# Kernel tuning notes

Measured on AMD Instinct MI355X. Metric: run time of the kernel, lower is better.

The kernel has to match this reference:

```python
import jax, jax.numpy as jnp
import numpy as np

WS = 8          # window_size
NH = 4          # num_heads
C = 128         # embed_dim
HD = C // NH    # head_dim
HID = 4 * C     # mlp hidden
EPS = 1e-5


def _rel_pos_index(ws):
    coords = np.stack(np.meshgrid(np.arange(ws), np.arange(ws), indexing='ij')).reshape(2, -1)
    rel = coords[:, :, None] - coords[:, None, :]          # (2, N, N)
    rel = rel.transpose(1, 2, 0).astype(np.int64)          # (N, N, 2)
    rel[..., 0] += ws - 1
    rel[..., 1] += ws - 1
    rel[..., 0] *= 2 * ws - 1
    return rel.sum(-1)                                     # (N, N)


def _layernorm(x, g, b):
    mu = jnp.mean(x, axis=-1, keepdims=True)
    var = jnp.mean(jnp.square(x - mu), axis=-1, keepdims=True)
    return (x - mu) * jax.lax.rsqrt(var + EPS) * g + b


def setup_inputs() -> dict:
    key = jax.random.key(0)
    ks = jax.random.split(key, 12)
    B, L = 32, 4096
    s = 0.02
    return {
        'x': jax.random.normal(ks[0], (B, L, C), jnp.float32),
        'W_qkv': jax.random.normal(ks[1], (C, 3 * C), jnp.float32) * s,
        'b_qkv': jnp.zeros((3 * C,), jnp.float32),
        'W_out': jax.random.normal(ks[2], (C, C), jnp.float32) * s,
        'b_out': jnp.zeros((C,), jnp.float32),
        'bias_table': jax.random.normal(ks[3], ((2 * WS - 1) ** 2, NH), jnp.float32) * s,
        'g1': jnp.ones((C,), jnp.float32), 'be1': jnp.zeros((C,), jnp.float32),
        'g2': jnp.ones((C,), jnp.float32), 'be2': jnp.zeros((C,), jnp.float32),
        'W_fc1': jax.random.normal(ks[4], (C, HID), jnp.float32) * s,
        'b_fc1': jnp.zeros((HID,), jnp.float32),
        'W_fc2': jax.random.normal(ks[5], (HID, C), jnp.float32) * s,
        'b_fc2': jnp.zeros((C,), jnp.float32),
        'H': 64, 'W': 64,
    }


def reference(x, W_qkv, b_qkv, W_out, b_out, bias_table, g1, be1, g2, be2,
              W_fc1, b_fc1, W_fc2, b_fc2, H, W):
    B, L, _ = x.shape
    N = WS * WS
    shortcut = x
    xn = _layernorm(x, g1, be1)
    # window partition: (B,H,W,C) -> (B*nw, N, C)
    xw = xn.reshape(B, H // WS, WS, W // WS, WS, C)
    xw = xw.transpose(0, 1, 3, 2, 4, 5).reshape(-1, N, C)
    # attention
    qkv = (xw @ W_qkv + b_qkv).reshape(-1, N, 3, NH, HD)
    q, k, v = jnp.moveaxis(qkv, 2, 0)                      # each (Bw, N, NH, HD)
    attn = jnp.einsum('bnhd,bmhd->bhnm', q, k) * (HD ** -0.5)
    idx = jnp.asarray(_rel_pos_index(WS))                  # (N, N)
    bias = bias_table[idx].transpose(2, 0, 1)              # (NH, N, N)
    attn = jax.nn.softmax((attn + bias[None]).astype(jnp.float32), axis=-1).astype(x.dtype)
    o = jnp.einsum('bhnm,bmhd->bnhd', attn, v).reshape(-1, N, C)
    o = o @ W_out + b_out
    # window reverse
    o = o.reshape(B, H // WS, W // WS, WS, WS, C)
    o = o.transpose(0, 1, 3, 2, 4, 5).reshape(B, L, C)
    x = shortcut + o
    # MLP block
    xn = _layernorm(x, g2, be2)
    h = jax.nn.gelu(xn @ W_fc1 + b_fc1, approximate=False)
    return x + (h @ W_fc2 + b_fc2)
```

## Files before the change

### kernel.cpp

```cpp
#include <hip/hip_runtime.h>
#include <hip/hip_bf16.h>

typedef __bf16 bf16;
typedef __bf16 bf16x8 __attribute__((ext_vector_type(8)));
typedef float f32x4 __attribute__((ext_vector_type(4)));

#define C_DIM 128
#define LDA 136
#define LDQ 40
#define LDVT 72
#define LDP 72
#define LDH 264

__device__ __forceinline__ f32x4 mfma16(bf16x8 a, bf16x8 b, f32x4 c) {
  return __builtin_amdgcn_mfma_f32_16x16x32_bf16(a, b, c, 0, 0, 0);
}


__global__ __launch_bounds__(256, 2) void swin_fused(
    const float* __restrict__ x,
    const bf16*  __restrict__ Wqkv_t, const float* __restrict__ b_qkv,
    const bf16*  __restrict__ Wout_t, const float* __restrict__ b_out,
    const float* __restrict__ btabx,
    const float* __restrict__ g1, const float* __restrict__ be1,
    const float* __restrict__ g2, const float* __restrict__ be2,
    const bf16*  __restrict__ Wfc1_t, const float* __restrict__ b_fc1,
    const bf16*  __restrict__ Wfc2_t, const float* __restrict__ b_fc2,
    float* __restrict__ out)
{
  __shared__ __attribute__((aligned(16))) char smem[76800];
  bf16 (*sA)[LDA]       = (bf16(*)[LDA])(smem);
  bf16 (*sQ)[64][LDQ]   = (bf16(*)[64][LDQ])(smem + 17408);
  bf16 (*sK)[64][LDQ]   = (bf16(*)[64][LDQ])(smem + 37888);
  bf16 (*sVT)[32][LDVT] = (bf16(*)[32][LDVT])(smem + 58368);
  bf16 (*sP)[64][LDP]   = (bf16(*)[64][LDP])(smem + 17408);
  bf16 (*sY)[LDA]       = (bf16(*)[LDA])(smem + 17408);
  bf16 (*sH)[LDH]       = (bf16(*)[LDH])(smem + 17408);

  const int tid = threadIdx.x;
  const int w   = tid >> 6;
  const int l   = tid & 63;
  const int l15 = l & 15;
  const int lhi = l >> 4;

  const int win = blockIdx.x;
  const int b   = win >> 6;
  const int wy  = (win >> 3) & 7;
  const int wx  = win & 7;
  const int rowbase = b * 4096 + wy * 512 + wx * 8;

  float yreg[2][4][4];

  {
    const int tok = tid >> 2, seg = tid & 3;
    const int t = rowbase + (tok >> 3) * 64 + (tok & 7);
    const float* xr = x + (size_t)t * C_DIM + seg * 32;
    float f[32]; float s = 0.f, s2 = 0.f;
    #pragma unroll
    for (int i = 0; i < 8; i++) {
      f32x4 v = *(const f32x4*)(xr + i * 4);
      #pragma unroll
      for (int j = 0; j < 4; j++) { float a = v[j]; f[i*4+j] = a; s += a; s2 += a*a; }
    }
    s  += __shfl_xor(s, 1);  s  += __shfl_xor(s, 2);
    s2 += __shfl_xor(s2, 1); s2 += __shfl_xor(s2, 2);
    float mu = s * (1.f/128.f);
    float rs = rsqrtf(s2 * (1.f/128.f) - mu*mu + 1e-5f);
    #pragma unroll
    for (int i = 0; i < 4; i++) {
      f32x4 gv0 = *(const f32x4*)(g1  + seg*32 + i*8);
      f32x4 gv1 = *(const f32x4*)(g1  + seg*32 + i*8 + 4);
      f32x4 bv0 = *(const f32x4*)(be1 + seg*32 + i*8);
      f32x4 bv1 = *(const f32x4*)(be1 + seg*32 + i*8 + 4);
      bf16x8 o;
      #pragma unroll
      for (int j = 0; j < 4; j++) {
        o[j]   = (bf16)((f[i*8+j]   - mu) * rs * gv0[j] + bv0[j]);
        o[j+4] = (bf16)((f[i*8+j+4] - mu) * rs * gv1[j] + bv1[j]);
      }
      *(bf16x8*)&sA[tok][seg*32 + i*8] = o;
    }
  }
  __syncthreads();

  {
    bf16x8 a[4][4];
    #pragma unroll
    for (int mt = 0; mt < 4; mt++)
      #pragma unroll
      for (int ks = 0; ks < 4; ks++)
        a[mt][ks] = *(const bf16x8*)&sA[mt*16 + l15][ks*32 + lhi*8];
    const float scale = 0.17677669529663687f;
    #pragma unroll
    for (int nti = 0; nti < 6; nti++) {
      const int kind = nti >> 1;
      const int d    = (nti & 1) * 16 + l15;
      const int colg = kind * 128 + w * 32 + d;
      const bf16* wp = Wqkv_t + (size_t)colg * 128 + lhi * 8;
      bf16x8 bw[4];
      #pragma unroll
      for (int ks = 0; ks < 4; ks++) bw[ks] = *(const bf16x8*)(wp + ks * 32);
      const float bias = b_qkv[colg];
      #pragma unroll
      for (int mt = 0; mt < 4; mt++) {
        f32x4 acc = {0.f, 0.f, 0.f, 0.f};
        #pragma unroll
        for (int ks = 0; ks < 4; ks++) acc = mfma16(a[mt][ks], bw[ks], acc);
        #pragma unroll
        for (int r = 0; r < 4; r++) {
          const int token = mt*16 + lhi*4 + r;
          float v = acc[r] + bias;
          if (kind == 0)      sQ[w][token][d] = (bf16)(v * scale);
          else if (kind == 1) sK[w][token][d] = (bf16)v;
          else                sVT[w][d][token] = (bf16)v;
        }
      }
    }
  }

  {
    const int h = w;
    bf16x8 aq[4], bk[4];
    #pragma unroll
    for (int mt = 0; mt < 4; mt++) aq[mt] = *(const bf16x8*)&sQ[h][mt*16 + l15][lhi*8];
    #pragma unroll
    for (int ct = 0; ct < 4; ct++) bk[ct] = *(const bf16x8*)&sK[h][ct*16 + l15][lhi*8];
    f32x4 sc[4][4];
    #pragma unroll
    for (int mt = 0; mt < 4; mt++)
      #pragma unroll
      for (int ct = 0; ct < 4; ct++) {
        f32x4 z = {0.f, 0.f, 0.f, 0.f};
        sc[mt][ct] = mfma16(aq[mt], bk[ct], z);
      }
    __syncthreads();
    #pragma unroll
    for (int mt = 0; mt < 4; mt++) {
      #pragma unroll
      for (int r = 0; r < 4; r++) {
        const int n = mt*16 + lhi*4 + r;
        f32x4 bv = *(const f32x4*)(btabx + (((h*64 + n)*16 + l15) << 2));
        float rv[4]; float sum = 0.f;
        #pragma unroll
        for (int ct = 0; ct < 4; ct++) { rv[ct] = __expf(sc[mt][ct][r] + bv[ct]); sum += rv[ct]; }
        #pragma unroll
        for (int o = 1; o < 16; o <<= 1) sum += __shfl_xor(sum, o);
        const float inv = 1.f / sum;
        #pragma unroll
        for (int ct = 0; ct < 4; ct++) sP[h][n][ct*16 + l15] = (bf16)(rv[ct] * inv);
      }
    }
    f32x4 o_[4][2];
    #pragma unroll
    for (int mt = 0; mt < 4; mt++) { f32x4 z = {0.f,0.f,0.f,0.f}; o_[mt][0] = z; o_[mt][1] = z; }
    #pragma unroll
    for (int ks = 0; ks < 2; ks++) {
      bf16x8 ap[4], bvv[2];
      #pragma unroll
      for (int mt = 0; mt < 4; mt++) ap[mt] = *(const bf16x8*)&sP[h][mt*16 + l15][ks*32 + lhi*8];
      #pragma unroll
      for (int c2 = 0; c2 < 2; c2++) bvv[c2] = *(const bf16x8*)&sVT[h][c2*16 + l15][ks*32 + lhi*8];
      #pragma unroll
      for (int mt = 0; mt < 4; mt++)
        #pragma unroll
        for (int c2 = 0; c2 < 2; c2++) o_[mt][c2] = mfma16(ap[mt], bvv[c2], o_[mt][c2]);
    }
    #pragma unroll
    for (int mt = 0; mt < 4; mt++)
      #pragma unroll
      for (int c2 = 0; c2 < 2; c2++)
        #pragma unroll
        for (int r = 0; r < 4; r++)
          sA[mt*16 + lhi*4 + r][h*32 + c2*16 + l15] = (bf16)o_[mt][c2][r];
  }
  __syncthreads();

  {
    bf16x8 a[4][4];
    #pragma unroll
    for (int mt = 0; mt < 4; mt++)
      #pragma unroll
      for (int ks = 0; ks < 4; ks++)
        a[mt][ks] = *(const bf16x8*)&sA[mt*16 + l15][ks*32 + lhi*8];
    #pragma unroll
    for (int nto = 0; nto < 2; nto++) {
      const int col = (w*2 + nto) * 16 + l15;
      const bf16* wp = Wout_t + (size_t)col * 128 + lhi * 8;
      bf16x8 bw[4];
      #pragma unroll
      for (int ks = 0; ks < 4; ks++) bw[ks] = *(const bf16x8*)(wp + ks * 32);
      const float bo = b_out[col];
      #pragma unroll
      for (int mt = 0; mt < 4; mt++) {
        f32x4 acc = {0.f, 0.f, 0.f, 0.f};
        #pragma unroll
        for (int ks = 0; ks < 4; ks++) acc = mfma16(a[mt][ks], bw[ks], acc);
        #pragma unroll
        for (int r = 0; r < 4; r++) {
          const int token = mt*16 + lhi*4 + r;
          const int t = rowbase + (token >> 3) * 64 + (token & 7);
          float v = acc[r] + bo + x[(size_t)t * C_DIM + col];
          yreg[nto][mt][r] = v;
          sY[token][col] = (bf16)v;
        }
      }
    }
  }
  __syncthreads();

  {
    const int tok = tid >> 2, seg = tid & 3;
    float f[32]; float s = 0.f, s2 = 0.f;
    #pragma unroll
    for (int i = 0; i < 4; i++) {
      bf16x8 v = *(const bf16x8*)&sY[tok][seg*32 + i*8];
      #pragma unroll
      for (int j = 0; j < 8; j++) { float a = (float)v[j]; f[i*8+j] = a; s += a; s2 += a*a; }
    }
    s  += __shfl_xor(s, 1);  s  += __shfl_xor(s, 2);
    s2 += __shfl_xor(s2, 1); s2 += __shfl_xor(s2, 2);
    float mu = s * (1.f/128.f);
    float rs = rsqrtf(s2 * (1.f/128.f) - mu*mu + 1e-5f);
    #pragma unroll
    for (int i = 0; i < 4; i++) {
      f32x4 gv0 = *(const f32x4*)(g2  + seg*32 + i*8);
      f32x4 gv1 = *(const f32x4*)(g2  + seg*32 + i*8 + 4);
      f32x4 bv0 = *(const f32x4*)(be2 + seg*32 + i*8);
      f32x4 bv1 = *(const f32x4*)(be2 + seg*32 + i*8 + 4);
      bf16x8 o;
      #pragma unroll
      for (int j = 0; j < 4; j++) {
        o[j]   = (bf16)((f[i*8+j]   - mu) * rs * gv0[j] + bv0[j]);
        o[j+4] = (bf16)((f[i*8+j+4] - mu) * rs * gv1[j] + bv1[j]);
      }
      *(bf16x8*)&sA[tok][seg*32 + i*8] = o;
    }
  }
  __syncthreads();

  {
    bf16x8 a[4][4];
    #pragma unroll
    for (int mt = 0; mt < 4; mt++)
      #pragma unroll
      for (int ks = 0; ks < 4; ks++)
        a[mt][ks] = *(const bf16x8*)&sA[mt*16 + l15][ks*32 + lhi*8];
    f32x4 accF[2][4];
    #pragma unroll
    for (int i = 0; i < 2; i++)
      #pragma unroll
      for (int mt = 0; mt < 4; mt++) { f32x4 z = {0.f,0.f,0.f,0.f}; accF[i][mt] = z; }

    #pragma unroll
    for (int hf = 0; hf < 2; hf++) {
      #pragma unroll
      for (int nti = 0; nti < 4; nti++) {
        const int ntg    = hf*16 + w*4 + nti;
        const int colh   = ntg*16 + l15;
        const int colloc = (w*4 + nti)*16 + l15;
        const bf16* wp = Wfc1_t + (size_t)colh * 128 + lhi * 8;
        bf16x8 bw[4];
        #pragma unroll
        for (int ks = 0; ks < 4; ks++) bw[ks] = *(const bf16x8*)(wp + ks * 32);
        const float bb = b_fc1[colh];
        #pragma unroll
        for (int mt = 0; mt < 4; mt++) {
          f32x4 acc = {0.f, 0.f, 0.f, 0.f};
          #pragma unroll
          for (int ks = 0; ks < 4; ks++) acc = mfma16(a[mt][ks], bw[ks], acc);
          #pragma unroll
          for (int r = 0; r < 4; r++) {
            float v = acc[r] + bb;
            float g = v / (1.f + __expf(-1.702f * v));
            sH[mt*16 + lhi*4 + r][colloc] = (bf16)g;
          }
        }
      }
      __syncthreads();
      #pragma unroll
      for (int ks = 0; ks < 8; ks++) {
        bf16x8 ah[4];
        #pragma unroll
        for (int mt = 0; mt < 4; mt++) ah[mt] = *(const bf16x8*)&sH[mt*16 + l15][ks*32 + lhi*8];
        #pragma unroll
        for (int nto = 0; nto < 2; nto++) {
          bf16x8 bw2 = *(const bf16x8*)(Wfc2_t + (size_t)((w*2 + nto)*16 + l15) * 512 + hf*256 + ks*32 + lhi*8);
          #pragma unroll
          for (int mt = 0; mt < 4; mt++) accF[nto][mt] = mfma16(ah[mt], bw2, accF[nto][mt]);
        }
      }
      __syncthreads();
    }
    #pragma unroll
    for (int nto = 0; nto < 2; nto++) {
      const int col = (w*2 + nto)*16 + l15;
      const float bb = b_fc2[col];
      #pragma unroll
      for (int mt = 0; mt < 4; mt++)
        #pragma unroll
        for (int r = 0; r < 4; r++) {
          const int token = mt*16 + lhi*4 + r;
          const int t = rowbase + (token >> 3) * 64 + (token & 7);
          out[(size_t)t * C_DIM + col] = accF[nto][mt][r] + bb + yreg[nto][mt][r];
        }
    }
  }
}

__global__ void prep_transpose(
    const float* __restrict__ Wqkv, const float* __restrict__ Wout,
    const float* __restrict__ Wfc1, const float* __restrict__ Wfc2,
    const float* __restrict__ btab,
    bf16* __restrict__ Wqkv_t, bf16* __restrict__ Wout_t,
    bf16* __restrict__ Wfc1_t, bf16* __restrict__ Wfc2_t,
    float* __restrict__ btabx)
{
  int i = blockIdx.x * 256 + threadIdx.x;
  if (i < 49152) { int n = i >> 7, k = i & 127; Wqkv_t[i] = (bf16)Wqkv[k*384 + n]; return; }
  i -= 49152;
  if (i < 16384) { int n = i >> 7, k = i & 127; Wout_t[i] = (bf16)Wout[k*128 + n]; return; }
  i -= 16384;
  if (i < 65536) { int n = i >> 7, k = i & 127; Wfc1_t[i] = (bf16)Wfc1[k*512 + n]; return; }
  i -= 65536;
  if (i < 65536) { int n = i >> 9, k = i & 511; Wfc2_t[i] = (bf16)Wfc2[k*128 + n]; return; }
  i -= 65536;
  if (i < 16384) {
    int ct  = i & 3;
    int l15 = (i >> 2) & 15;
    int n   = (i >> 6) & 63;
    int h   = i >> 12;
    int m = ct * 16 + l15;
    int nr = n >> 3, nc = n & 7, mr = m >> 3, mc = m & 7;
    int idx = (nr - mr + 7) * 15 + (nc - mc + 7);
    btabx[i] = btab[idx * 4 + h];
  }
}

extern "C" void kernel_launch(void* const* d_in, const int* in_sizes, int n_in,
                              void* d_out, int out_size, void* d_ws, size_t ws_size,
                              hipStream_t stream)
{
  const float* x    = (const float*)d_in[0];
  const float* Wqkv = (const float*)d_in[1];
  const float* bqkv = (const float*)d_in[2];
  const float* Wout = (const float*)d_in[3];
  const float* bout = (const float*)d_in[4];
  const float* btab = (const float*)d_in[5];
  const float* g1   = (const float*)d_in[6];
  const float* be1  = (const float*)d_in[7];
  const float* g2   = (const float*)d_in[8];
  const float* be2  = (const float*)d_in[9];
  const float* Wfc1 = (const float*)d_in[10];
  const float* bfc1 = (const float*)d_in[11];
  const float* Wfc2 = (const float*)d_in[12];
  const float* bfc2 = (const float*)d_in[13];

  bf16* ws = (bf16*)d_ws;
  bf16* Wqkv_t = ws;
  bf16* Wout_t = ws + 49152;
  bf16* Wfc1_t = ws + 65536;
  bf16* Wfc2_t = ws + 131072;
  float* btabx = (float*)(ws + 196608);

  prep_transpose<<<832, 256, 0, stream>>>(Wqkv, Wout, Wfc1, Wfc2, btab,
                                          Wqkv_t, Wout_t, Wfc1_t, Wfc2_t, btabx);

  const int B = in_sizes[0] / (4096 * 128);
  swin_fused<<<dim3(B * 64), 256, 0, stream>>>(
      x, Wqkv_t, bqkv, Wout_t, bout, btabx, g1, be1, g2, be2,
      Wfc1_t, bfc1, Wfc2_t, bfc2, (float*)d_out);
}
```

Measured before the change: 167.6 us.

## Swap MFMA operand order so accumulators hold contiguous columns for vector stores

Every MFMA now takes the weight or K/V fragment as the A operand and the activation as the B operand. Each lane's four accumulator values then cover four consecutive output columns for a single token rather than four tokens. This turns the per-element bf16 stores to shared memory and the fp32 residual loads and output stores into 4-wide vector accesses, and lets biases load as f32x4. The softmax row reduction becomes two cross-lane shuffles, and the bias table is re-laid out to match the new fragment mapping. The V transpose store remains scalar.

```diff
diff --git a/kernel.cpp b/kernel.cpp
--- a/kernel.cpp
+++ b/kernel.cpp
@@ -3,6 +3,7 @@
 
 typedef __bf16 bf16;
 typedef __bf16 bf16x8 __attribute__((ext_vector_type(8)));
+typedef __bf16 bf16x4 __attribute__((ext_vector_type(4)));
 typedef float f32x4 __attribute__((ext_vector_type(4)));
 
 #define C_DIM 128
@@ -49,7 +50,7 @@
   const int wx  = win & 7;
   const int rowbase = b * 4096 + wy * 512 + wx * 8;
 
-  float yreg[2][4][4];
+  f32x4 yreg[2][4];
 
   {
     const int tok = tid >> 2, seg = tid & 3;
@@ -93,26 +94,35 @@
     const float scale = 0.17677669529663687f;
     #pragma unroll
     for (int nti = 0; nti < 6; nti++) {
-      const int kind = nti >> 1;
-      const int d    = (nti & 1) * 16 + l15;
-      const int colg = kind * 128 + w * 32 + d;
-      const bf16* wp = Wqkv_t + (size_t)colg * 128 + lhi * 8;
+      const int kind  = nti >> 1;
+      const int dhalf = nti & 1;
+      const int colg_l = kind*128 + w*32 + dhalf*16 + l15;
+      const bf16* wp = Wqkv_t + (size_t)colg_l * 128 + lhi * 8;
       bf16x8 bw[4];
       #pragma unroll
       for (int ks = 0; ks < 4; ks++) bw[ks] = *(const bf16x8*)(wp + ks * 32);
-      const float bias = b_qkv[colg];
+      const int colg_o = kind*128 + w*32 + dhalf*16 + lhi*4;
+      f32x4 bias4 = *(const f32x4*)(b_qkv + colg_o);
+      const int d_base = dhalf*16 + lhi*4;
       #pragma unroll
       for (int mt = 0; mt < 4; mt++) {
         f32x4 acc = {0.f, 0.f, 0.f, 0.f};
         #pragma unroll
-        for (int ks = 0; ks < 4; ks++) acc = mfma16(a[mt][ks], bw[ks], acc);
-        #pragma unroll
-        for (int r = 0; r < 4; r++) {
-          const int token = mt*16 + lhi*4 + r;
-          float v = acc[r] + bias;
-          if (kind == 0)      sQ[w][token][d] = (bf16)(v * scale);
-          else if (kind == 1) sK[w][token][d] = (bf16)v;
-          else                sVT[w][d][token] = (bf16)v;
+        for (int ks = 0; ks < 4; ks++) acc = mfma16(bw[ks], a[mt][ks], acc);
+        const int token = mt*16 + l15;
+        if (kind == 0) {
+          bf16x4 v4;
+          #pragma unroll
+          for (int r = 0; r < 4; r++) v4[r] = (bf16)((acc[r] + bias4[r]) * scale);
+          *(bf16x4*)&sQ[w][token][d_base] = v4;
+        } else if (kind == 1) {
+          bf16x4 v4;
+          #pragma unroll
+          for (int r = 0; r < 4; r++) v4[r] = (bf16)(acc[r] + bias4[r]);
+          *(bf16x4*)&sK[w][token][d_base] = v4;
+        } else {
+          #pragma unroll
+          for (int r = 0; r < 4; r++) sVT[w][d_base + r][token] = (bf16)(acc[r] + bias4[r]);
         }
       }
     }
@@ -120,58 +130,67 @@
 
   {
     const int h = w;
-    bf16x8 aq[4], bk[4];
-    #pragma unroll
-    for (int mt = 0; mt < 4; mt++) aq[mt] = *(const bf16x8*)&sQ[h][mt*16 + l15][lhi*8];
-    #pragma unroll
-    for (int ct = 0; ct < 4; ct++) bk[ct] = *(const bf16x8*)&sK[h][ct*16 + l15][lhi*8];
+    bf16x8 qf[4], kf[4];
+    #pragma unroll
+    for (int ctq = 0; ctq < 4; ctq++) qf[ctq] = *(const bf16x8*)&sQ[h][ctq*16 + l15][lhi*8];
+    #pragma unroll
+    for (int kt = 0; kt < 4; kt++) kf[kt] = *(const bf16x8*)&sK[h][kt*16 + l15][lhi*8];
     f32x4 sc[4][4];
     #pragma unroll
-    for (int mt = 0; mt < 4; mt++)
-      #pragma unroll
-      for (int ct = 0; ct < 4; ct++) {
+    for (int ctq = 0; ctq < 4; ctq++)
+      #pragma unroll
+      for (int kt = 0; kt < 4; kt++) {
         f32x4 z = {0.f, 0.f, 0.f, 0.f};
-        sc[mt][ct] = mfma16(aq[mt], bk[ct], z);
+        sc[ctq][kt] = mfma16(kf[kt], qf[ctq], z);
       }
     __syncthreads();
     #pragma unroll
-    for (int mt = 0; mt < 4; mt++) {
-      #pragma unroll
-      for (int r = 0; r < 4; r++) {
-        const int n = mt*16 + lhi*4 + r;
-        f32x4 bv = *(const f32x4*)(btabx + (((h*64 + n)*16 + l15) << 2));
-        float rv[4]; float sum = 0.f;
-        #pragma unroll
-        for (int ct = 0; ct < 4; ct++) { rv[ct] = __expf(sc[mt][ct][r] + bv[ct]); sum += rv[ct]; }
-        #pragma unroll
-        for (int o = 1; o < 16; o <<= 1) sum += __shfl_xor(sum, o);
-        const float inv = 1.f / sum;
-        #pragma unroll
-        for (int ct = 0; ct < 4; ct++) sP[h][n][ct*16 + l15] = (bf16)(rv[ct] * inv);
-      }
-    }
-    f32x4 o_[4][2];
-    #pragma unroll
-    for (int mt = 0; mt < 4; mt++) { f32x4 z = {0.f,0.f,0.f,0.f}; o_[mt][0] = z; o_[mt][1] = z; }
+    for (int ctq = 0; ctq < 4; ctq++) {
+      const int q = ctq*16 + l15;
+      float e[4][4]; float loc = 0.f;
+      #pragma unroll
+      for (int kt = 0; kt < 4; kt++) {
+        f32x4 bt = *(const f32x4*)(btabx + (size_t)(((h*64 + q)*16 + kt*4 + lhi) << 2));
+        #pragma unroll
+        for (int r = 0; r < 4; r++) { e[kt][r] = __expf(sc[ctq][kt][r] + bt[r]); loc += e[kt][r]; }
+      }
+      loc += __shfl_xor(loc, 16);
+      loc += __shfl_xor(loc, 32);
+      const float inv = 1.f / loc;
+      #pragma unroll
+      for (int kt = 0; kt < 4; kt++) {
+        bf16x4 p4;
+        #pragma unroll
+        for (int r = 0; r < 4; r++) p4[r] = (bf16)(e[kt][r] * inv);
+        *(bf16x4*)&sP[h][q][kt*16 + lhi*4] = p4;
+      }
+    }
+    f32x4 o_[2][4];
+    #pragma unroll
+    for (int c2 = 0; c2 < 2; c2++)
+      #pragma unroll
+      for (int ctq = 0; ctq < 4; ctq++) { f32x4 z = {0.f,0.f,0.f,0.f}; o_[c2][ctq] = z; }
     #pragma unroll
     for (int ks = 0; ks < 2; ks++) {
-      bf16x8 ap[4], bvv[2];
-      #pragma unroll
-      for (int mt = 0; mt < 4; mt++) ap[mt] = *(const bf16x8*)&sP[h][mt*16 + l15][ks*32 + lhi*8];
-      #pragma unroll
-      for (int c2 = 0; c2 < 2; c2++) bvv[c2] = *(const bf16x8*)&sVT[h][c2*16 + l15][ks*32 + lhi*8];
-      #pragma unroll
-      for (int mt = 0; mt < 4; mt++)
-        #pragma unroll
-        for (int c2 = 0; c2 < 2; c2++) o_[mt][c2] = mfma16(ap[mt], bvv[c2], o_[mt][c2]);
-    }
-    #pragma unroll
-    for (int mt = 0; mt < 4; mt++)
+      bf16x8 vf[2], pq[4];
+      #pragma unroll
+      for (int c2 = 0; c2 < 2; c2++) vf[c2] = *(const bf16x8*)&sVT[h][c2*16 + l15][ks*32 + lhi*8];
+      #pragma unroll
+      for (int ctq = 0; ctq < 4; ctq++) pq[ctq] = *(const bf16x8*)&sP[h][ctq*16 + l15][ks*32 + lhi*8];
       #pragma unroll
       for (int c2 = 0; c2 < 2; c2++)
         #pragma unroll
-        for (int r = 0; r < 4; r++)
-          sA[mt*16 + lhi*4 + r][h*32 + c2*16 + l15] = (bf16)o_[mt][c2][r];
+        for (int ctq = 0; ctq < 4; ctq++) o_[c2][ctq] = mfma16(vf[c2], pq[ctq], o_[c2][ctq]);
+    }
+    #pragma unroll
+    for (int c2 = 0; c2 < 2; c2++)
+      #pragma unroll
+      for (int ctq = 0; ctq < 4; ctq++) {
+        bf16x4 o4;
+        #pragma unroll
+        for (int r = 0; r < 4; r++) o4[r] = (bf16)o_[c2][ctq][r];
+        *(bf16x4*)&sA[ctq*16 + l15][h*32 + c2*16 + lhi*4] = o4;
+      }
   }
   __syncthreads();
 
@@ -184,25 +203,26 @@
         a[mt][ks] = *(const bf16x8*)&sA[mt*16 + l15][ks*32 + lhi*8];
     #pragma unroll
     for (int nto = 0; nto < 2; nto++) {
-      const int col = (w*2 + nto) * 16 + l15;
-      const bf16* wp = Wout_t + (size_t)col * 128 + lhi * 8;
+      const int col_l = (w*2 + nto) * 16 + l15;
+      const bf16* wp = Wout_t + (size_t)col_l * 128 + lhi * 8;
       bf16x8 bw[4];
       #pragma unroll
       for (int ks = 0; ks < 4; ks++) bw[ks] = *(const bf16x8*)(wp + ks * 32);
-      const float bo = b_out[col];
+      const int col_o = (w*2 + nto) * 16 + lhi*4;
+      f32x4 bo4 = *(const f32x4*)(b_out + col_o);
       #pragma unroll
       for (int mt = 0; mt < 4; mt++) {
         f32x4 acc = {0.f, 0.f, 0.f, 0.f};
         #pragma unroll
-        for (int ks = 0; ks < 4; ks++) acc = mfma16(a[mt][ks], bw[ks], acc);
-        #pragma unroll
-        for (int r = 0; r < 4; r++) {
-          const int token = mt*16 + lhi*4 + r;
-          const int t = rowbase + (token >> 3) * 64 + (token & 7);
-          float v = acc[r] + bo + x[(size_t)t * C_DIM + col];
-          yreg[nto][mt][r] = v;
-          sY[token][col] = (bf16)v;
-        }
+        for (int ks = 0; ks < 4; ks++) acc = mfma16(bw[ks], a[mt][ks], acc);
+        const int token = mt*16 + l15;
+        const int t = rowbase + (token >> 3) * 64 + (token & 7);
+        f32x4 xv = *(const f32x4*)(x + (size_t)t * C_DIM + col_o);
+        f32x4 yv; bf16x4 y4;
+        #pragma unroll
+        for (int r = 0; r < 4; r++) { yv[r] = acc[r] + bo4[r] + xv[r]; y4[r] = (bf16)yv[r]; }
+        yreg[nto][mt] = yv;
+        *(bf16x4*)&sY[token][col_o] = y4;
       }
     }
   }
@@ -256,24 +276,27 @@
       #pragma unroll
       for (int nti = 0; nti < 4; nti++) {
         const int ntg    = hf*16 + w*4 + nti;
-        const int colh   = ntg*16 + l15;
-        const int colloc = (w*4 + nti)*16 + l15;
-        const bf16* wp = Wfc1_t + (size_t)colh * 128 + lhi * 8;
+        const int colh_l = ntg*16 + l15;
+        const bf16* wp = Wfc1_t + (size_t)colh_l * 128 + lhi * 8;
         bf16x8 bw[4];
         #pragma unroll
         for (int ks = 0; ks < 4; ks++) bw[ks] = *(const bf16x8*)(wp + ks * 32);
-        const float bb = b_fc1[colh];
+        const int colh_o = ntg*16 + lhi*4;
+        f32x4 bb4 = *(const f32x4*)(b_fc1 + colh_o);
+        const int colloc_o = (w*4 + nti)*16 + lhi*4;
         #pragma unroll
         for (int mt = 0; mt < 4; mt++) {
           f32x4 acc = {0.f, 0.f, 0.f, 0.f};
           #pragma unroll
-          for (int ks = 0; ks < 4; ks++) acc = mfma16(a[mt][ks], bw[ks], acc);
+          for (int ks = 0; ks < 4; ks++) acc = mfma16(bw[ks], a[mt][ks], acc);
+          const int token = mt*16 + l15;
+          bf16x4 h4;
           #pragma unroll
           for (int r = 0; r < 4; r++) {
-            float v = acc[r] + bb;
-            float g = v / (1.f + __expf(-1.702f * v));
-            sH[mt*16 + lhi*4 + r][colloc] = (bf16)g;
+            float v = acc[r] + bb4[r];
+            h4[r] = (bf16)(v / (1.f + __expf(-1.702f * v)));
           }
+          *(bf16x4*)&sH[token][colloc_o] = h4;
         }
       }
       __syncthreads();
@@ -286,23 +309,24 @@
         for (int nto = 0; nto < 2; nto++) {
           bf16x8 bw2 = *(const bf16x8*)(Wfc2_t + (size_t)((w*2 + nto)*16 + l15) * 512 + hf*256 + ks*32 + lhi*8);
           #pragma unroll
-          for (int mt = 0; mt < 4; mt++) accF[nto][mt] = mfma16(ah[mt], bw2, accF[nto][mt]);
+          for (int mt = 0; mt < 4; mt++) accF[nto][mt] = mfma16(bw2, ah[mt], accF[nto][mt]);
         }
       }
       __syncthreads();
     }
     #pragma unroll
     for (int nto = 0; nto < 2; nto++) {
-      const int col = (w*2 + nto)*16 + l15;
-      const float bb = b_fc2[col];
-      #pragma unroll
-      for (int mt = 0; mt < 4; mt++)
-        #pragma unroll
-        for (int r = 0; r < 4; r++) {
-          const int token = mt*16 + lhi*4 + r;
-          const int t = rowbase + (token >> 3) * 64 + (token & 7);
-          out[(size_t)t * C_DIM + col] = accF[nto][mt][r] + bb + yreg[nto][mt][r];
-        }
+      const int col_o = (w*2 + nto)*16 + lhi*4;
+      f32x4 bb = *(const f32x4*)(b_fc2 + col_o);
+      #pragma unroll
+      for (int mt = 0; mt < 4; mt++) {
+        const int token = mt*16 + l15;
+        const int t = rowbase + (token >> 3) * 64 + (token & 7);
+        f32x4 ov;
+        #pragma unroll
+        for (int r = 0; r < 4; r++) ov[r] = accF[nto][mt][r] + bb[r] + yreg[nto][mt][r];
+        *(f32x4*)(out + (size_t)t * C_DIM + col_o) = ov;
+      }
     }
   }
 }
@@ -325,12 +349,13 @@
   if (i < 65536) { int n = i >> 9, k = i & 511; Wfc2_t[i] = (bf16)Wfc2[k*128 + n]; return; }
   i -= 65536;
   if (i < 16384) {
-    int ct  = i & 3;
-    int l15 = (i >> 2) & 15;
-    int n   = (i >> 6) & 63;
+    int r   = i & 3;
+    int lhi = (i >> 2) & 3;
+    int kt  = (i >> 4) & 3;
+    int q   = (i >> 6) & 63;
     int h   = i >> 12;
-    int m = ct * 16 + l15;
-    int nr = n >> 3, nc = n & 7, mr = m >> 3, mc = m & 7;
+    int k = kt*16 + lhi*4 + r;
+    int nr = q >> 3, nc = q & 7, mr = k >> 3, mc = k & 7;
     int idx = (nr - mr + 7) * 15 + (nc - mc + 7);
     btabx[i] = btab[idx * 4 + h];
   }
```

Result: slower. 172.4 us (+2.9%).
